# Optimization experiments

Hardware: AMD Instinct MI355X
Metric: run time of the kernel (lower is better)

## Reference

```python
import jax, jax.numpy as jnp
import numpy as np

B, S, D, H, NI, NB = 512, 200, 256, 4, 100000, 2
DH = D // H
NEG = float(-(2**32) + 1)
SCALE = float(1.0 / np.sqrt(DH))


def ln(x, g, b, eps=1e-3):
    # keras LayerNormalization (default epsilon=1e-3)
    m = jnp.mean(x, axis=-1, keepdims=True)
    v = jnp.var(x, axis=-1, keepdims=True)
    return (x - m) * jax.lax.rsqrt(v + eps) * g + b


def setup_inputs() -> dict:
    key = jax.random.key(0)
    ks = jax.random.split(key, 10)
    s = 0.02
    return {
        "input_ids": jax.random.randint(ks[0], (B, S), 0, NI + 1, dtype=jnp.int32),
        "item_emb": jax.random.normal(ks[1], (NI + 1, D), jnp.float32) * s,
        "pos_emb": jax.random.normal(ks[2], (S, D), jnp.float32) * s,
        "ln1_g": jnp.ones((NB, D), jnp.float32),
        "ln1_b": jnp.zeros((NB, D), jnp.float32),
        "wq": jax.random.normal(ks[3], (NB, D, D), jnp.float32) * s,
        "bq": jnp.zeros((NB, D), jnp.float32),
        "wk": jax.random.normal(ks[4], (NB, D, D), jnp.float32) * s,
        "bk": jnp.zeros((NB, D), jnp.float32),
        "wv": jax.random.normal(ks[5], (NB, D, D), jnp.float32) * s,
        "bv": jnp.zeros((NB, D), jnp.float32),
        "ln2_g": jnp.ones((NB, D), jnp.float32),
        "ln2_b": jnp.zeros((NB, D), jnp.float32),
        "wd": jax.random.normal(ks[6], (NB, D, D), jnp.float32) * s,
        "bd": jnp.zeros((NB, D), jnp.float32),
        "seq_g": jnp.ones((D,), jnp.float32),
        "seq_b": jnp.zeros((D,), jnp.float32),
        "out_item_emb": jax.random.normal(ks[7], (NI, D), jnp.float32) * s,
    }


def reference(input_ids, item_emb, pos_emb, ln1_g, ln1_b, wq, bq, wk, bk, wv, bv,
              ln2_g, ln2_b, wd, bd, seq_g, seq_b, out_item_emb):
    seq = item_emb[input_ids] + pos_emb[None]                      # [B,S,D]
    mask = (input_ids != NI).astype(seq.dtype)[:, :, None]        # pad id == num_items
    causal = jnp.tril(jnp.ones((S, S), bool))
    for i in range(NB):
        x = ln(seq, ln1_g[i], ln1_b[i])                            # queries (pre-norm)
        q = (x @ wq[i] + bq[i]).reshape(B, S, H, DH).transpose(0, 2, 1, 3)
        k = (seq @ wk[i] + bk[i]).reshape(B, S, H, DH).transpose(0, 2, 1, 3)
        v = (seq @ wv[i] + bv[i]).reshape(B, S, H, DH).transpose(0, 2, 1, 3)
        scores = jnp.einsum('bhqd,bhkd->bhqk', q, k) * SCALE       # [B,H,S,S]
        scores = jnp.where(causal, scores, NEG)
        attn = jax.nn.softmax(scores, axis=-1)
        o = jnp.einsum('bhqk,bhkd->bhqd', attn, v)
        o = o.transpose(0, 2, 1, 3).reshape(B, S, D)
        x2 = o + x                                                 # residual to normed queries
        y = jax.nn.relu(ln(x2, ln2_g[i], ln2_b[i]) @ wd[i] + bd[i])
        seq = (y + x2) * mask
    seq_emb = ln(seq[:, -1, :], seq_g, seq_b)                      # [B,D]
    return seq_emb @ out_item_emb.T                                # [B,num_items], linear act
```

## Files before the change

kernel.cpp:

```cpp
#include <hip/hip_runtime.h>
#include <hip/hip_bf16.h>
#include <cstdint>
#include <cstddef>

namespace {
constexpr int B = 512, S = 200, D = 256, H = 4, DH = 64, NI = 100000;
constexpr float EPS = 1e-3f;
constexpr float SCALE = 0.125f;
}

typedef __attribute__((ext_vector_type(8))) short bf16x8;
typedef __attribute__((ext_vector_type(4))) float f32x4;

__device__ inline unsigned short f2b(float f) {
  union { float f; unsigned int u; } v; v.f = f;
  unsigned int r = v.u + 0x7FFFu + ((v.u >> 16) & 1u);
  return (unsigned short)(r >> 16);
}

__device__ inline float b2f(unsigned short u) {
  union { unsigned int i; float f; } x; x.i = (unsigned int)u << 16; return x.f;
}

__device__ inline bf16x8 pack8(float4 a, float4 b) {
  bf16x8 r;
  r[0] = (short)f2b(a.x); r[1] = (short)f2b(a.y); r[2] = (short)f2b(a.z); r[3] = (short)f2b(a.w);
  r[4] = (short)f2b(b.x); r[5] = (short)f2b(b.y); r[6] = (short)f2b(b.z); r[7] = (short)f2b(b.w);
  return r;
}

__device__ inline ushort4 pack4(float4 a) {
  ushort4 r;
  r.x = f2b(a.x); r.y = f2b(a.y); r.z = f2b(a.z); r.w = f2b(a.w);
  return r;
}

__device__ inline float4 unpack4(ushort4 u) {
  float4 r; r.x = b2f(u.x); r.y = b2f(u.y); r.z = b2f(u.z); r.w = b2f(u.w); return r;
}

__device__ inline void gload_lds16(const unsigned short* g, unsigned short* l) {
  __builtin_amdgcn_global_load_lds((const __attribute__((address_space(1))) void*)g,
                                   (__attribute__((address_space(3))) void*)l, 16, 0, 0);
}

__global__ void cvt_wt_k(const float* __restrict__ wq, const float* __restrict__ wk,
                         const float* __restrict__ wv, const float* __restrict__ wd,
                         unsigned short* __restrict__ dst) {
  const int t = blockIdx.x * 256 + threadIdx.x;
  const int w = t >> 14, rem = t & 16383;
  const int k = rem >> 6, n4 = (rem & 63) * 4;
  const int blk = w >> 2, which = w & 3;
  const float* src = (which == 0 ? wq : which == 1 ? wk : which == 2 ? wv : wd) + blk * 65536;
  const float4 v = *(const float4*)(src + k * 256 + n4);
  unsigned short* d = dst + w * 65536;
  d[(n4 + 0) * 256 + k] = f2b(v.x);
  d[(n4 + 1) * 256 + k] = f2b(v.y);
  d[(n4 + 2) * 256 + k] = f2b(v.z);
  d[(n4 + 3) * 256 + k] = f2b(v.w);
}

__global__ __launch_bounds__(256) void embed_ln_k(const int* __restrict__ ids,
                                                  const float* __restrict__ ie,
                                                  const float* __restrict__ pe,
                                                  const float* __restrict__ g1,
                                                  const float* __restrict__ b1,
                                                  unsigned short* __restrict__ seq_bf,
                                                  unsigned short* __restrict__ x_bf) {
  const int row = blockIdx.x * 4 + (threadIdx.x >> 6);
  const int lane = threadIdx.x & 63;
  const int id = ids[row];
  const int s = row % S;
  float4 v = *(const float4*)(ie + (size_t)id * D + (lane << 2));
  const float4 p = *(const float4*)(pe + (size_t)s * D + (lane << 2));
  v.x += p.x; v.y += p.y; v.z += p.z; v.w += p.w;
  *(ushort4*)(seq_bf + (size_t)row * D + (lane << 2)) = pack4(v);
  const float4 vb = unpack4(pack4(v));
  float su = vb.x + vb.y + vb.z + vb.w;
  float ss = vb.x * vb.x + vb.y * vb.y + vb.z * vb.z + vb.w * vb.w;
#pragma unroll
  for (int off = 32; off; off >>= 1) {
    su += __shfl_xor(su, off);
    ss += __shfl_xor(ss, off);
  }
  const float mean = su * (1.f / D);
  const float rs = rsqrtf(ss * (1.f / D) - mean * mean + EPS);
  const float4 gv = *(const float4*)(g1 + (lane << 2));
  const float4 bv = *(const float4*)(b1 + (lane << 2));
  float4 o;
  o.x = (vb.x - mean) * rs * gv.x + bv.x;
  o.y = (vb.y - mean) * rs * gv.y + bv.y;
  o.z = (vb.z - mean) * rs * gv.z + bv.z;
  o.w = (vb.w - mean) * rs * gv.w + bv.w;
  *(ushort4*)(x_bf + (size_t)row * D + (lane << 2)) = pack4(o);
}

__global__ __launch_bounds__(256) void ln_bf_k(const unsigned short* __restrict__ in,
                                               size_t in_stride,
                                               const float* __restrict__ g, const float* __restrict__ b,
                                               unsigned short* __restrict__ outp, int nrows) {
  const int row = blockIdx.x * 4 + (threadIdx.x >> 6);
  if (row >= nrows) return;
  const int lane = threadIdx.x & 63;
  const float4 v = unpack4(*(const ushort4*)(in + (size_t)row * in_stride + (lane << 2)));
  float s = v.x + v.y + v.z + v.w;
  float ss = v.x * v.x + v.y * v.y + v.z * v.z + v.w * v.w;
#pragma unroll
  for (int off = 32; off; off >>= 1) {
    s += __shfl_xor(s, off);
    ss += __shfl_xor(ss, off);
  }
  const float mean = s * (1.f / D);
  const float rs = rsqrtf(ss * (1.f / D) - mean * mean + EPS);
  const float4 gv = *(const float4*)(g + (lane << 2));
  const float4 bv = *(const float4*)(b + (lane << 2));
  float4 o;
  o.x = (v.x - mean) * rs * gv.x + bv.x;
  o.y = (v.y - mean) * rs * gv.y + bv.y;
  o.z = (v.z - mean) * rs * gv.z + bv.z;
  o.w = (v.w - mean) * rs * gv.w + bv.w;
  *(ushort4*)(outp + (size_t)row * D + (lane << 2)) = pack4(o);
}

__global__ __launch_bounds__(256) void ln2x2_k(const unsigned short* __restrict__ x_bf,
                                               const unsigned short* __restrict__ o_bf,
                                               const float* __restrict__ g2, const float* __restrict__ b2,
                                               unsigned short* __restrict__ x2b,
                                               unsigned short* __restrict__ t_bf, int nrows) {
  const int row = blockIdx.x * 4 + (threadIdx.x >> 6);
  if (row >= nrows) return;
  const int lane = threadIdx.x & 63;
  const float4 xv = unpack4(*(const ushort4*)(x_bf + (size_t)row * D + (lane << 2)));
  const float4 ov = unpack4(*(const ushort4*)(o_bf + (size_t)row * D + (lane << 2)));
  float4 x2;
  x2.x = xv.x + ov.x; x2.y = xv.y + ov.y; x2.z = xv.z + ov.z; x2.w = xv.w + ov.w;
  *(ushort4*)(x2b + (size_t)row * D + (lane << 2)) = pack4(x2);
  float s2 = x2.x + x2.y + x2.z + x2.w;
  float ss2 = x2.x * x2.x + x2.y * x2.y + x2.z * x2.z + x2.w * x2.w;
#pragma unroll
  for (int off = 32; off; off >>= 1) {
    s2 += __shfl_xor(s2, off);
    ss2 += __shfl_xor(ss2, off);
  }
  const float mean2 = s2 * (1.f / D);
  const float rs2 = rsqrtf(ss2 * (1.f / D) - mean2 * mean2 + EPS);
  const float4 g2v = *(const float4*)(g2 + (lane << 2));
  const float4 b2v = *(const float4*)(b2 + (lane << 2));
  float4 t;
  t.x = (x2.x - mean2) * rs2 * g2v.x + b2v.x;
  t.y = (x2.y - mean2) * rs2 * g2v.y + b2v.y;
  t.z = (x2.z - mean2) * rs2 * g2v.z + b2v.z;
  t.w = (x2.w - mean2) * rs2 * g2v.w + b2v.w;
  *(ushort4*)(t_bf + (size_t)row * D + (lane << 2)) = pack4(t);
}

template <int RELU, int UPD, int LN1>
__global__ __launch_bounds__(512) void bgemm2_k(const unsigned short* __restrict__ A,
                                                const unsigned short* __restrict__ Wt,
                                                const float* __restrict__ bias,
                                                unsigned short* __restrict__ Cbf,
                                                const unsigned short* __restrict__ x2b,
                                                const int* __restrict__ ids, float osc,
                                                const float* __restrict__ g1,
                                                const float* __restrict__ b1,
                                                unsigned short* __restrict__ x1) {
  __shared__ unsigned short As[128 * 64];
  __shared__ unsigned short Bs[256 * 64];
  const int tid = threadIdx.x, w = tid >> 6, lane = tid & 63;
  const int kb = lane >> 4, ln = lane & 15;
  const int m0 = blockIdx.x * 128;
  const int wm = w & 1, wn = w >> 1;

  f32x4 acc[4][4];
#pragma unroll
  for (int i = 0; i < 4; ++i)
#pragma unroll
    for (int j = 0; j < 4; ++j) acc[i][j] = (f32x4){0.f, 0.f, 0.f, 0.f};

  for (int ks = 0; ks < 4; ++ks) {
    const int ko = ks * 64;
#pragma unroll
    for (int r = 0; r < 2; ++r) {
      const int g = (w * 2 + r) * 64 + lane;
      const int row = g >> 3, gc = g & 7;
      gload_lds16(A + (size_t)(m0 + row) * 256 + ko + ((gc ^ (row & 7)) << 3),
                  As + (size_t)(w * 2 + r) * 512);
    }
#pragma unroll
    for (int r = 0; r < 4; ++r) {
      const int g = (w * 4 + r) * 64 + lane;
      const int row = g >> 3, gc = g & 7;
      gload_lds16(Wt + (size_t)row * 256 + ko + ((gc ^ (row & 7)) << 3),
                  Bs + (size_t)(w * 4 + r) * 512);
    }
    __syncthreads();
#pragma unroll
    for (int h = 0; h < 2; ++h) {
      bf16x8 af[4], bfr[4];
#pragma unroll
      for (int i = 0; i < 4; ++i) {
        const int ar = wm * 64 + i * 16 + ln;
        af[i] = *(const bf16x8*)(As + ar * 64 + (((h * 64 + kb * 16) ^ ((ar & 7) << 4)) >> 1));
        const int br = wn * 64 + i * 16 + ln;
        bfr[i] = *(const bf16x8*)(Bs + br * 64 + (((h * 64 + kb * 16) ^ ((br & 7) << 4)) >> 1));
      }
#pragma unroll
      for (int i = 0; i < 4; ++i)
#pragma unroll
        for (int j = 0; j < 4; ++j)
          acc[i][j] = __builtin_amdgcn_mfma_f32_16x16x32_bf16(af[i], bfr[j], acc[i][j], 0, 0, 0);
    }
    __syncthreads();
  }

  const int crow0 = m0 + wm * 64 + kb * 4;
  const int ccol0 = wn * 64 + ln;
  float mk[4][4];
  if (UPD) {
#pragma unroll
    for (int i = 0; i < 4; ++i)
#pragma unroll
      for (int r = 0; r < 4; ++r) mk[i][r] = (ids[crow0 + i * 16 + r] != NI) ? 1.f : 0.f;
  }
#pragma unroll
  for (int j = 0; j < 4; ++j) {
    const int col = ccol0 + j * 16;
    const float bj = bias[col];
#pragma unroll
    for (int i = 0; i < 4; ++i) {
#pragma unroll
      for (int r = 0; r < 4; ++r) {
        const int row = crow0 + i * 16 + r;
        float v = (acc[i][j][r] + bj) * osc;
        if (RELU) v = fmaxf(v, 0.f);
        if (UPD) v = (v + b2f(x2b[(size_t)row * 256 + col])) * mk[i][r];
        const unsigned short vb = f2b(v);
        Cbf[(size_t)row * 256 + col] = vb;
        if (LN1) acc[i][j][r] = b2f(vb);
      }
    }
  }

  if (LN1) {
    float s_[4][4], ss_[4][4];
#pragma unroll
    for (int i = 0; i < 4; ++i)
#pragma unroll
      for (int r = 0; r < 4; ++r) {
        float s = 0.f, ss = 0.f;
#pragma unroll
        for (int j = 0; j < 4; ++j) { const float v = acc[i][j][r]; s += v; ss += v * v; }
#pragma unroll
        for (int off = 1; off < 16; off <<= 1) {
          s += __shfl_xor(s, off);
          ss += __shfl_xor(ss, off);
        }
        s_[i][r] = s; ss_[i][r] = ss;
      }
    float* red = (float*)As;
    if (ln == 0) {
#pragma unroll
      for (int i = 0; i < 4; ++i)
#pragma unroll
        for (int r = 0; r < 4; ++r) {
          const int rl = wm * 64 + kb * 4 + i * 16 + r;
          red[rl * 8 + wn * 2 + 0] = s_[i][r];
          red[rl * 8 + wn * 2 + 1] = ss_[i][r];
        }
    }
    __syncthreads();
#pragma unroll
    for (int i = 0; i < 4; ++i)
#pragma unroll
      for (int r = 0; r < 4; ++r) {
        const int rl = wm * 64 + kb * 4 + i * 16 + r;
        float S = 0.f, SS = 0.f;
#pragma unroll
        for (int q = 0; q < 4; ++q) { S += red[rl * 8 + q * 2]; SS += red[rl * 8 + q * 2 + 1]; }
        const float mean = S * (1.f / D);
        s_[i][r] = mean;
        ss_[i][r] = rsqrtf(SS * (1.f / D) - mean * mean + EPS);
      }
#pragma unroll
    for (int j = 0; j < 4; ++j) {
      const int col = ccol0 + j * 16;
      const float gc = g1[col], bc = b1[col];
#pragma unroll
      for (int i = 0; i < 4; ++i) {
#pragma unroll
        for (int r = 0; r < 4; ++r) {
          const int row = crow0 + i * 16 + r;
          const float xv = (acc[i][j][r] - s_[i][r]) * ss_[i][r] * gc + bc;
          x1[(size_t)row * 256 + col] = f2b(xv);
        }
      }
    }
  }
}

__global__ __launch_bounds__(256) void bgemm3_k(const unsigned short* __restrict__ A,
                                                const float* __restrict__ Wf,
                                                float* __restrict__ C, int M, int N) {
  __shared__ unsigned short As[128 * 64];
  __shared__ unsigned short Bs[128 * 64];
  const int tid = threadIdx.x, w = tid >> 6, lane = tid & 63;
  const int kb = lane >> 4, ln = lane & 15;
  const int m0 = blockIdx.x * 128;
  const int n0 = blockIdx.y * 128;
  const int wm = w & 1, wn = w >> 1;
  const int rl = lane >> 3;
  const int cb = (lane & 7) << 4;

  f32x4 acc[4][4];
#pragma unroll
  for (int i = 0; i < 4; ++i)
#pragma unroll
    for (int j = 0; j < 4; ++j) acc[i][j] = (f32x4){0.f, 0.f, 0.f, 0.f};

  for (int ks = 0; ks < 4; ++ks) {
    const int ko = ks * 64;
#pragma unroll
    for (int c = 0; c < 4; ++c) {
      const int arow = w * 32 + c * 8 + rl;
      const int sw = (arow & 7) << 4;
      const int cu = (cb ^ sw) >> 1;
      gload_lds16(A + (size_t)(m0 + arow) * 256 + ko + cu, As + (w * 32 + c * 8) * 64);
    }
#pragma unroll
    for (int c = 0; c < 4; ++c) {
      const int g = c * 256 + tid;
      const int row = g >> 3, gcs = g & 7;
      int br = n0 + row; if (br > N - 1) br = N - 1;
      const float* src = Wf + (size_t)br * 256 + ko + gcs * 8;
      const float4 f0 = *(const float4*)src;
      const float4 f1 = *(const float4*)(src + 4);
      *(bf16x8*)(Bs + row * 64 + ((gcs ^ (row & 7)) << 3)) = pack8(f0, f1);
    }
    __syncthreads();
#pragma unroll
    for (int h = 0; h < 2; ++h) {
      bf16x8 af[4], bfr[4];
#pragma unroll
      for (int i = 0; i < 4; ++i) {
        const int ar = wm * 64 + i * 16 + ln;
        af[i] = *(const bf16x8*)(As + ar * 64 + (((h * 64 + kb * 16) ^ ((ar & 7) << 4)) >> 1));
        const int br = wn * 64 + i * 16 + ln;
        bfr[i] = *(const bf16x8*)(Bs + br * 64 + (((h * 64 + kb * 16) ^ ((br & 7) << 4)) >> 1));
      }
#pragma unroll
      for (int i = 0; i < 4; ++i)
#pragma unroll
        for (int j = 0; j < 4; ++j)
          acc[i][j] = __builtin_amdgcn_mfma_f32_16x16x32_bf16(af[i], bfr[j], acc[i][j], 0, 0, 0);
    }
    __syncthreads();
  }

  const int crow0 = m0 + wm * 64 + kb * 4;
  const int ccol0 = n0 + wn * 64 + ln;
#pragma unroll
  for (int j = 0; j < 4; ++j) {
    const int col = ccol0 + j * 16;
    if (col >= N) continue;
#pragma unroll
    for (int i = 0; i < 4; ++i) {
#pragma unroll
      for (int r = 0; r < 4; ++r) {
        const int row = crow0 + i * 16 + r;
        C[(size_t)row * N + col] = acc[i][j][r];
      }
    }
  }
}

__global__ __launch_bounds__(256) void attn_k(const unsigned short* __restrict__ Q,
                                              const unsigned short* __restrict__ Kg,
                                              const unsigned short* __restrict__ Vg,
                                              unsigned short* __restrict__ O) {
  __shared__ unsigned short Ks[13312];
  __shared__ unsigned short Vt[13312];
  __shared__ unsigned short Ps[4 * 3328];
  const int b = blockIdx.x >> 2;
  const int h = blockIdx.x & 3;
  const int tid = threadIdx.x, w = tid >> 6, lane = tid & 63;
  const int kb = lane >> 4, ln = lane & 15;
  const size_t base = (size_t)b * S * D + h * DH;

  for (int s = w; s < 26; s += 4) {
    const int t = s >> 1, h2 = s & 1;
    int krow = t * 16 + ln; if (krow > S - 1) krow = S - 1;
    gload_lds16(Kg + base + (size_t)krow * D + h2 * 32 + kb * 8, Ks + s * 512);
  }
  for (int g = tid; g < 200 * 8; g += 256) {
    const int key = g >> 3, d0 = (g & 7) * 8;
    const bf16x8 v = *(const bf16x8*)(Vg + base + (size_t)key * D + d0);
#pragma unroll
    for (int i = 0; i < 8; ++i) {
      const int d = d0 + i, ct = d >> 4, cl = d & 15;
      int addr;
      if (key < 192) addr = (((ct * 6 + (key >> 5)) * 4 + ((key >> 3) & 3)) * 16 + cl) * 8 + (key & 7);
      else           addr = 12288 + ((ct * 2 + ((key >> 3) & 1)) * 16 + cl) * 8 + (key & 7);
      Vt[addr] = (unsigned short)v[i];
    }
  }
  if (tid < 64) {
    const int ct = tid >> 4, cl = tid & 15;
    *(bf16x8*)(Vt + 12288 + ((ct * 2 + 1) * 16 + cl) * 8) = (bf16x8)0;
  }
  __syncthreads();
  unsigned short* Pw = Ps + w * 3328;

#pragma unroll
  for (int it = 0; it < 4; ++it) {
    const int c = (it == 0) ? (12 - w) : (it == 1) ? (5 + w) : (it == 2) ? (4 - w)
                                                                         : (w == 3 ? 0 : -1);
    if (c < 0) continue;
    const int q0 = c << 4;
    const int tmax = (c | 1) > 12 ? 12 : (c | 1);
    const int ktm = c >> 1;

    int qr = q0 + ln; if (qr > S - 1) qr = S - 1;
    const unsigned short* qp = Q + base + (size_t)qr * D + kb * 8;
    const bf16x8 aq0 = *(const bf16x8*)(qp);
    const bf16x8 aq1 = *(const bf16x8*)(qp + 32);
    f32x4 sc[13];
#pragma unroll
    for (int t = 0; t < 13; ++t) {
      if (t <= tmax) {
        f32x4 a = {0.f, 0.f, 0.f, 0.f};
        a = __builtin_amdgcn_mfma_f32_16x16x32_bf16(aq0, *(const bf16x8*)(Ks + (t * 2 + 0) * 512 + lane * 8), a, 0, 0, 0);
        a = __builtin_amdgcn_mfma_f32_16x16x32_bf16(aq1, *(const bf16x8*)(Ks + (t * 2 + 1) * 512 + lane * 8), a, 0, 0, 0);
        sc[t] = a;
      }
    }
    float inv[4];
#pragma unroll
    for (int r = 0; r < 4; ++r) {
      const int q = q0 + kb * 4 + r;
      const int qrow = kb * 4 + r;
      float m = -1e30f;
#pragma unroll
      for (int t = 0; t < 13; ++t) {
        if (t <= tmax) {
          const int j = t * 16 + ln;
          float s = sc[t][r];
          s = (j <= q) ? s : -1e30f;
          sc[t][r] = s;
          m = fmaxf(m, s);
        }
      }
      m = fmaxf(m, __shfl_xor(m, 1));
      m = fmaxf(m, __shfl_xor(m, 2));
      m = fmaxf(m, __shfl_xor(m, 4));
      m = fmaxf(m, __shfl_xor(m, 8));
      float sm = 0.f;
#pragma unroll
      for (int t = 0; t < 13; ++t) {
        if (t <= tmax) {
          const float e = __expf(sc[t][r] - m);
          sm += e;
          int addr;
          if (t < 12) addr = (((t >> 1) * 4 + ((2 * t + (ln >> 3)) & 3)) * 16 + qrow) * 8 + (ln & 7);
          else        addr = 3072 + ((ln >> 3) * 16 + qrow) * 8 + (ln & 7);
          Pw[addr] = f2b(e);
        }
      }
      sm += __shfl_xor(sm, 1);
      sm += __shfl_xor(sm, 2);
      sm += __shfl_xor(sm, 4);
      sm += __shfl_xor(sm, 8);
      inv[r] = 1.f / sm;
    }
#pragma unroll
    for (int ct = 0; ct < 4; ++ct) {
      f32x4 a = {0.f, 0.f, 0.f, 0.f};
#pragma unroll
      for (int kt = 0; kt < 6; ++kt) {
        if (kt <= ktm) {
          const bf16x8 pa = *(const bf16x8*)(Pw + ((kt * 4 + kb) * 16 + ln) * 8);
          const bf16x8 vb = *(const bf16x8*)(Vt + (((ct * 6 + kt) * 4 + kb) * 16 + ln) * 8);
          a = __builtin_amdgcn_mfma_f32_16x16x32_bf16(pa, vb, a, 0, 0, 0);
        }
      }
      if (c == 12) {
        bf16x8 pa = (bf16x8)0, vb = (bf16x8)0;
        if (kb < 2) {
          pa = *(const bf16x8*)(Pw + 3072 + (kb * 16 + ln) * 8);
          vb = *(const bf16x8*)(Vt + 12288 + ((ct * 2 + kb) * 16 + ln) * 8);
        }
        a = __builtin_amdgcn_mfma_f32_16x16x32_bf16(pa, vb, a, 0, 0, 0);
      }
#pragma unroll
      for (int r = 0; r < 4; ++r) {
        const int q = q0 + kb * 4 + r;
        if (q < S) O[base + (size_t)q * D + ct * 16 + ln] = f2b(a[r] * inv[r]);
      }
    }
  }
}

extern "C" void kernel_launch(void* const* d_in, const int* in_sizes, int n_in,
                              void* d_out, int out_size, void* d_ws, size_t ws_size,
                              hipStream_t stream) {
  const int* ids        = (const int*)d_in[0];
  const float* item_emb = (const float*)d_in[1];
  const float* pos_emb  = (const float*)d_in[2];
  const float* ln1_g    = (const float*)d_in[3];
  const float* ln1_b    = (const float*)d_in[4];
  const float* wq       = (const float*)d_in[5];
  const float* bq       = (const float*)d_in[6];
  const float* wk       = (const float*)d_in[7];
  const float* bk       = (const float*)d_in[8];
  const float* wv       = (const float*)d_in[9];
  const float* bv       = (const float*)d_in[10];
  const float* ln2_g    = (const float*)d_in[11];
  const float* ln2_b    = (const float*)d_in[12];
  const float* wd       = (const float*)d_in[13];
  const float* bd       = (const float*)d_in[14];
  const float* seq_g    = (const float*)d_in[15];
  const float* seq_b    = (const float*)d_in[16];
  const float* w_out    = (const float*)d_in[17];
  float* out = (float*)d_out;

  char* wsb = (char*)d_ws;
  unsigned short* seq_bf = (unsigned short*)(wsb + 0);
  unsigned short* x_bf   = (unsigned short*)(wsb + 52428800);
  unsigned short* q_bf   = (unsigned short*)(wsb + 104857600);
  unsigned short* k_bf   = (unsigned short*)(wsb + 157286400);
  unsigned short* v_bf   = (unsigned short*)(wsb + 209715200);
  unsigned short* o_bf   = (unsigned short*)(wsb + 262144000);
  unsigned short* x2b    = (unsigned short*)(wsb + 314572800);
  unsigned short* wtb    = (unsigned short*)(wsb + 367001600);
  unsigned short* semb   = (unsigned short*)(wsb + 368050176);

  const int M = B * S;
  const int ln_grid = (M + 3) / 4;

  cvt_wt_k<<<512, 256, 0, stream>>>(wq, wk, wv, wd, wtb);
  embed_ln_k<<<ln_grid, 256, 0, stream>>>(ids, item_emb, pos_emb, ln1_g, ln1_b, seq_bf, x_bf);

  for (int blk = 0; blk < 2; ++blk) {
    const float* l2g = ln2_g + blk * D;
    const float* l2b = ln2_b + blk * D;
    const unsigned short* WT = wtb + (size_t)blk * 4 * 65536;

    bgemm2_k<0, 0, 0><<<800, 512, 0, stream>>>(seq_bf, WT + 1 * 65536, bk + blk * D, k_bf,
                                               nullptr, nullptr, 1.f, nullptr, nullptr, nullptr);
    bgemm2_k<0, 0, 0><<<800, 512, 0, stream>>>(seq_bf, WT + 2 * 65536, bv + blk * D, v_bf,
                                               nullptr, nullptr, 1.f, nullptr, nullptr, nullptr);
    bgemm2_k<0, 0, 0><<<800, 512, 0, stream>>>(x_bf, WT + 0 * 65536, bq + blk * D, q_bf,
                                               nullptr, nullptr, SCALE, nullptr, nullptr, nullptr);
    attn_k<<<B * H, 256, 0, stream>>>(q_bf, k_bf, v_bf, o_bf);
    ln2x2_k<<<ln_grid, 256, 0, stream>>>(x_bf, o_bf, l2g, l2b, x2b, q_bf, M);
    if (blk == 0) {
      bgemm2_k<1, 1, 1><<<800, 512, 0, stream>>>(q_bf, WT + 3 * 65536, bd + blk * D, seq_bf,
                                                 x2b, ids, 1.f, ln1_g + D, ln1_b + D, x_bf);
    } else {
      bgemm2_k<1, 1, 0><<<800, 512, 0, stream>>>(q_bf, WT + 3 * 65536, bd + blk * D, seq_bf,
                                                 x2b, ids, 1.f, nullptr, nullptr, nullptr);
    }
  }

  ln_bf_k<<<(B + 3) / 4, 256, 0, stream>>>(seq_bf + (size_t)(S - 1) * D, (size_t)S * D,
                                           seq_g, seq_b, semb, B);
  bgemm3_k<<<dim3(4, 782), 256, 0, stream>>>(semb, w_out, out, B, NI);
}
```

Baseline: 780.7 us.

## Fuse residual and LN2 into FFN GEMM; restructure logits GEMM to load weights once

The separate residual-add and LayerNorm-2 kernel is folded into a new FFN kernel. That kernel builds x2 = x + o for a 64-row tile in shared memory, normalizes it in place, and then runs the dense GEMM with the ReLU, residual, mask and optional next LN1 epilogue. This removes the x2 and t intermediates from global memory and one launch per block. The output-projection GEMM is also restructured so that each block converts a 128-row slice of the fp32 item embedding to bf16 once and loops over all 512 batch rows. Previously each weight tile was re-read and re-converted for each of four M tiles. The new kernels use much larger shared memory, 128 KB for the logits kernel, which lowers occupancy.

```diff
diff --git a/kernel.cpp b/kernel.cpp
--- a/kernel.cpp
+++ b/kernel.cpp
@@ -122,48 +122,10 @@
   *(ushort4*)(outp + (size_t)row * D + (lane << 2)) = pack4(o);
 }
 
-__global__ __launch_bounds__(256) void ln2x2_k(const unsigned short* __restrict__ x_bf,
-                                               const unsigned short* __restrict__ o_bf,
-                                               const float* __restrict__ g2, const float* __restrict__ b2,
-                                               unsigned short* __restrict__ x2b,
-                                               unsigned short* __restrict__ t_bf, int nrows) {
-  const int row = blockIdx.x * 4 + (threadIdx.x >> 6);
-  if (row >= nrows) return;
-  const int lane = threadIdx.x & 63;
-  const float4 xv = unpack4(*(const ushort4*)(x_bf + (size_t)row * D + (lane << 2)));
-  const float4 ov = unpack4(*(const ushort4*)(o_bf + (size_t)row * D + (lane << 2)));
-  float4 x2;
-  x2.x = xv.x + ov.x; x2.y = xv.y + ov.y; x2.z = xv.z + ov.z; x2.w = xv.w + ov.w;
-  *(ushort4*)(x2b + (size_t)row * D + (lane << 2)) = pack4(x2);
-  float s2 = x2.x + x2.y + x2.z + x2.w;
-  float ss2 = x2.x * x2.x + x2.y * x2.y + x2.z * x2.z + x2.w * x2.w;
-#pragma unroll
-  for (int off = 32; off; off >>= 1) {
-    s2 += __shfl_xor(s2, off);
-    ss2 += __shfl_xor(ss2, off);
-  }
-  const float mean2 = s2 * (1.f / D);
-  const float rs2 = rsqrtf(ss2 * (1.f / D) - mean2 * mean2 + EPS);
-  const float4 g2v = *(const float4*)(g2 + (lane << 2));
-  const float4 b2v = *(const float4*)(b2 + (lane << 2));
-  float4 t;
-  t.x = (x2.x - mean2) * rs2 * g2v.x + b2v.x;
-  t.y = (x2.y - mean2) * rs2 * g2v.y + b2v.y;
-  t.z = (x2.z - mean2) * rs2 * g2v.z + b2v.z;
-  t.w = (x2.w - mean2) * rs2 * g2v.w + b2v.w;
-  *(ushort4*)(t_bf + (size_t)row * D + (lane << 2)) = pack4(t);
-}
-
-template <int RELU, int UPD, int LN1>
 __global__ __launch_bounds__(512) void bgemm2_k(const unsigned short* __restrict__ A,
                                                 const unsigned short* __restrict__ Wt,
                                                 const float* __restrict__ bias,
-                                                unsigned short* __restrict__ Cbf,
-                                                const unsigned short* __restrict__ x2b,
-                                                const int* __restrict__ ids, float osc,
-                                                const float* __restrict__ g1,
-                                                const float* __restrict__ b1,
-                                                unsigned short* __restrict__ x1) {
+                                                unsigned short* __restrict__ Cbf, float osc) {
   __shared__ unsigned short As[128 * 64];
   __shared__ unsigned short Bs[256 * 64];
   const int tid = threadIdx.x, w = tid >> 6, lane = tid & 63;
@@ -215,13 +177,6 @@
 
   const int crow0 = m0 + wm * 64 + kb * 4;
   const int ccol0 = wn * 64 + ln;
-  float mk[4][4];
-  if (UPD) {
-#pragma unroll
-    for (int i = 0; i < 4; ++i)
-#pragma unroll
-      for (int r = 0; r < 4; ++r) mk[i][r] = (ids[crow0 + i * 16 + r] != NI) ? 1.f : 0.f;
-  }
 #pragma unroll
   for (int j = 0; j < 4; ++j) {
     const int col = ccol0 + j * 16;
@@ -231,16 +186,156 @@
 #pragma unroll
       for (int r = 0; r < 4; ++r) {
         const int row = crow0 + i * 16 + r;
-        float v = (acc[i][j][r] + bj) * osc;
-        if (RELU) v = fmaxf(v, 0.f);
-        if (UPD) v = (v + b2f(x2b[(size_t)row * 256 + col])) * mk[i][r];
+        Cbf[(size_t)row * 256 + col] = f2b((acc[i][j][r] + bj) * osc);
+      }
+    }
+  }
+}
+
+template <int LN1>
+__global__ __launch_bounds__(256) void ffn_k(const unsigned short* __restrict__ x_bf,
+                                             const unsigned short* __restrict__ o_bf,
+                                             const unsigned short* __restrict__ Wt,
+                                             const float* __restrict__ bias,
+                                             const float* __restrict__ g2,
+                                             const float* __restrict__ b2,
+                                             const int* __restrict__ ids,
+                                             unsigned short* __restrict__ seq_out,
+                                             const float* __restrict__ g1,
+                                             const float* __restrict__ b1,
+                                             unsigned short* __restrict__ x1) {
+  __shared__ unsigned short Xt[64 * 256];
+  __shared__ unsigned short Bs[256 * 64];
+  __shared__ float stats[64][2];
+  __shared__ float params[512];
+  const int tid = threadIdx.x, w = tid >> 6, lane = tid & 63;
+  const int kb = lane >> 4, ln = lane & 15;
+  const int m0 = blockIdx.x * 64;
+  const int wn = w;
+
+  params[tid] = g2[tid & 255];
+  params[256 + (tid & 255)] = b2[tid & 255];
+#pragma unroll
+  for (int it = 0; it < 8; ++it) {
+    const int g = it * 256 + tid;
+    const int row = g >> 5, gc = g & 31;
+    const bf16x8 xv = *(const bf16x8*)(x_bf + (size_t)(m0 + row) * 256 + gc * 8);
+    const bf16x8 ov = *(const bf16x8*)(o_bf + (size_t)(m0 + row) * 256 + gc * 8);
+    bf16x8 sv;
+#pragma unroll
+    for (int e = 0; e < 8; ++e)
+      sv[e] = (short)f2b(b2f((unsigned short)xv[e]) + b2f((unsigned short)ov[e]));
+    *(bf16x8*)(Xt + row * 256 + (((gc * 16) ^ ((row & 7) << 4)) >> 1)) = sv;
+  }
+  __syncthreads();
+  {
+    const int srow = tid >> 2, sq = tid & 3;
+    float su = 0.f, ssq = 0.f;
+#pragma unroll
+    for (int gg = 0; gg < 8; ++gg) {
+      const int gc = sq * 8 + gg;
+      const bf16x8 v = *(const bf16x8*)(Xt + srow * 256 + (((gc * 16) ^ ((srow & 7) << 4)) >> 1));
+#pragma unroll
+      for (int e = 0; e < 8; ++e) {
+        const float f = b2f((unsigned short)v[e]);
+        su += f; ssq += f * f;
+      }
+    }
+    su += __shfl_xor(su, 1); ssq += __shfl_xor(ssq, 1);
+    su += __shfl_xor(su, 2); ssq += __shfl_xor(ssq, 2);
+    if (sq == 0) {
+      const float mean = su * (1.f / D);
+      stats[srow][0] = mean;
+      stats[srow][1] = rsqrtf(ssq * (1.f / D) - mean * mean + EPS);
+    }
+  }
+  __syncthreads();
+  float ep[4][4][4];
+  const int ccl = wn * 64 + ln;
+#pragma unroll
+  for (int i = 0; i < 4; ++i)
+#pragma unroll
+    for (int j = 0; j < 4; ++j)
+#pragma unroll
+      for (int r = 0; r < 4; ++r) {
+        const int rr = i * 16 + kb * 4 + r;
+        const int col = ccl + j * 16;
+        ep[i][j][r] = b2f(Xt[rr * 256 + (((col * 2) ^ ((rr & 7) << 4)) >> 1)]);
+      }
+  __syncthreads();
+#pragma unroll
+  for (int it = 0; it < 8; ++it) {
+    const int g = it * 256 + tid;
+    const int row = g >> 5, gc = g & 31;
+    const int idx = row * 256 + (((gc * 16) ^ ((row & 7) << 4)) >> 1);
+    const bf16x8 v = *(const bf16x8*)(Xt + idx);
+    const float mu = stats[row][0], rs = stats[row][1];
+    bf16x8 t;
+#pragma unroll
+    for (int e = 0; e < 8; ++e) {
+      const int k = gc * 8 + e;
+      t[e] = (short)f2b((b2f((unsigned short)v[e]) - mu) * rs * params[k] + params[256 + k]);
+    }
+    *(bf16x8*)(Xt + idx) = t;
+  }
+  __syncthreads();
+  f32x4 acc[4][4];
+#pragma unroll
+  for (int i = 0; i < 4; ++i)
+#pragma unroll
+    for (int j = 0; j < 4; ++j) acc[i][j] = (f32x4){0.f, 0.f, 0.f, 0.f};
+
+  for (int ks = 0; ks < 4; ++ks) {
+#pragma unroll
+    for (int r = 0; r < 8; ++r) {
+      const int g = (w * 8 + r) * 64 + lane;
+      const int row = g >> 3, gc = g & 7;
+      gload_lds16(Wt + (size_t)row * 256 + ks * 64 + ((gc ^ (row & 7)) << 3),
+                  Bs + (size_t)(w * 8 + r) * 512);
+    }
+    __syncthreads();
+#pragma unroll
+    for (int h = 0; h < 2; ++h) {
+      bf16x8 af[4], bfr[4];
+#pragma unroll
+      for (int i = 0; i < 4; ++i) {
+        const int ar = i * 16 + ln;
+        af[i] = *(const bf16x8*)(Xt + ar * 256 +
+                                 ((ks * 128 + ((h * 64 + kb * 16) ^ ((ar & 7) << 4))) >> 1));
+        const int br = wn * 64 + i * 16 + ln;
+        bfr[i] = *(const bf16x8*)(Bs + br * 64 + (((h * 64 + kb * 16) ^ ((br & 7) << 4)) >> 1));
+      }
+#pragma unroll
+      for (int i = 0; i < 4; ++i)
+#pragma unroll
+        for (int j = 0; j < 4; ++j)
+          acc[i][j] = __builtin_amdgcn_mfma_f32_16x16x32_bf16(af[i], bfr[j], acc[i][j], 0, 0, 0);
+    }
+    __syncthreads();
+  }
+  float mk[4][4];
+#pragma unroll
+  for (int i = 0; i < 4; ++i)
+#pragma unroll
+    for (int r = 0; r < 4; ++r)
+      mk[i][r] = (ids[m0 + i * 16 + kb * 4 + r] != NI) ? 1.f : 0.f;
+#pragma unroll
+  for (int j = 0; j < 4; ++j) {
+    const int col = ccl + j * 16;
+    const float bj = bias[col];
+#pragma unroll
+    for (int i = 0; i < 4; ++i) {
+#pragma unroll
+      for (int r = 0; r < 4; ++r) {
+        const int grow = m0 + i * 16 + kb * 4 + r;
+        float v = fmaxf(acc[i][j][r] + bj, 0.f);
+        v = (v + ep[i][j][r]) * mk[i][r];
         const unsigned short vb = f2b(v);
-        Cbf[(size_t)row * 256 + col] = vb;
+        seq_out[(size_t)grow * 256 + col] = vb;
         if (LN1) acc[i][j][r] = b2f(vb);
       }
     }
   }
-
   if (LN1) {
     float s_[4][4], ss_[4][4];
 #pragma unroll
@@ -257,15 +352,16 @@
         }
         s_[i][r] = s; ss_[i][r] = ss;
       }
-    float* red = (float*)As;
+    float* red = params;
+    __syncthreads();
     if (ln == 0) {
 #pragma unroll
       for (int i = 0; i < 4; ++i)
 #pragma unroll
         for (int r = 0; r < 4; ++r) {
-          const int rl = wm * 64 + kb * 4 + i * 16 + r;
-          red[rl * 8 + wn * 2 + 0] = s_[i][r];
-          red[rl * 8 + wn * 2 + 1] = ss_[i][r];
+          const int rt = i * 16 + kb * 4 + r;
+          red[rt * 8 + wn * 2 + 0] = s_[i][r];
+          red[rt * 8 + wn * 2 + 1] = ss_[i][r];
         }
     }
     __syncthreads();
@@ -273,103 +369,102 @@
     for (int i = 0; i < 4; ++i)
 #pragma unroll
       for (int r = 0; r < 4; ++r) {
-        const int rl = wm * 64 + kb * 4 + i * 16 + r;
-        float S = 0.f, SS = 0.f;
-#pragma unroll
-        for (int q = 0; q < 4; ++q) { S += red[rl * 8 + q * 2]; SS += red[rl * 8 + q * 2 + 1]; }
-        const float mean = S * (1.f / D);
+        const int rt = i * 16 + kb * 4 + r;
+        float Sv = 0.f, SS = 0.f;
+#pragma unroll
+        for (int q = 0; q < 4; ++q) { Sv += red[rt * 8 + q * 2]; SS += red[rt * 8 + q * 2 + 1]; }
+        const float mean = Sv * (1.f / D);
         s_[i][r] = mean;
         ss_[i][r] = rsqrtf(SS * (1.f / D) - mean * mean + EPS);
       }
 #pragma unroll
     for (int j = 0; j < 4; ++j) {
+      const int col = ccl + j * 16;
+      const float gc = g1[col], bc = b1[col];
+#pragma unroll
+      for (int i = 0; i < 4; ++i) {
+#pragma unroll
+        for (int r = 0; r < 4; ++r) {
+          const int grow = m0 + i * 16 + kb * 4 + r;
+          const float xv = (acc[i][j][r] - s_[i][r]) * ss_[i][r] * gc + bc;
+          x1[(size_t)grow * 256 + col] = f2b(xv);
+        }
+      }
+    }
+  }
+}
+
+__global__ __launch_bounds__(256) void logits_k(const unsigned short* __restrict__ A,
+                                                const float* __restrict__ Wf,
+                                                float* __restrict__ C) {
+  __shared__ unsigned short Bs[128 * 256];
+  __shared__ unsigned short As[128 * 256];
+  const int tid = threadIdx.x, w = tid >> 6, lane = tid & 63;
+  const int kb = lane >> 4, ln = lane & 15;
+  const int wm = w & 1, wn = w >> 1;
+  const int n0 = blockIdx.x * 128;
+#pragma unroll
+  for (int it = 0; it < 16; ++it) {
+    const int g = it * 256 + tid;
+    const int row = g >> 5, gc = g & 31;
+    int br = n0 + row; if (br > NI - 1) br = NI - 1;
+    const float* src = Wf + (size_t)br * 256 + gc * 8;
+    const float4 f0 = *(const float4*)src;
+    const float4 f1 = *(const float4*)(src + 4);
+    *(bf16x8*)(Bs + row * 256 + (((gc * 16) ^ ((row & 7) << 4)) >> 1)) = pack8(f0, f1);
+  }
+  for (int m = 0; m < 4; ++m) {
+    const int m0 = m * 128;
+#pragma unroll
+    for (int it = 0; it < 16; ++it) {
+      const int g = it * 256 + w * 64 + lane;
+      const int row = g >> 5, gc = g & 31;
+      gload_lds16(A + (size_t)(m0 + row) * 256 + (((gc * 16) ^ ((row & 7) << 4)) >> 1),
+                  As + (size_t)(it * 256 + w * 64) * 8);
+    }
+    __syncthreads();
+    f32x4 acc[4][4];
+#pragma unroll
+    for (int i = 0; i < 4; ++i)
+#pragma unroll
+      for (int j = 0; j < 4; ++j) acc[i][j] = (f32x4){0.f, 0.f, 0.f, 0.f};
+#pragma unroll
+    for (int ks = 0; ks < 4; ++ks) {
+#pragma unroll
+      for (int h = 0; h < 2; ++h) {
+        bf16x8 af[4], bfr[4];
+#pragma unroll
+        for (int i = 0; i < 4; ++i) {
+          const int ar = wm * 64 + i * 16 + ln;
+          af[i] = *(const bf16x8*)(As + ar * 256 +
+                                   ((ks * 128 + ((h * 64 + kb * 16) ^ ((ar & 7) << 4))) >> 1));
+          const int br = wn * 64 + i * 16 + ln;
+          bfr[i] = *(const bf16x8*)(Bs + br * 256 +
+                                    ((ks * 128 + ((h * 64 + kb * 16) ^ ((br & 7) << 4))) >> 1));
+        }
+#pragma unroll
+        for (int i = 0; i < 4; ++i)
+#pragma unroll
+          for (int j = 0; j < 4; ++j)
+            acc[i][j] = __builtin_amdgcn_mfma_f32_16x16x32_bf16(af[i], bfr[j], acc[i][j], 0, 0, 0);
+      }
+    }
+    const int crow0 = m0 + wm * 64 + kb * 4;
+    const int ccol0 = n0 + wn * 64 + ln;
+#pragma unroll
+    for (int j = 0; j < 4; ++j) {
       const int col = ccol0 + j * 16;
-      const float gc = g1[col], bc = b1[col];
+      if (col >= NI) continue;
 #pragma unroll
       for (int i = 0; i < 4; ++i) {
 #pragma unroll
         for (int r = 0; r < 4; ++r) {
           const int row = crow0 + i * 16 + r;
-          const float xv = (acc[i][j][r] - s_[i][r]) * ss_[i][r] * gc + bc;
-          x1[(size_t)row * 256 + col] = f2b(xv);
-        }
-      }
-    }
-  }
-}
-
-__global__ __launch_bounds__(256) void bgemm3_k(const unsigned short* __restrict__ A,
-                                                const float* __restrict__ Wf,
-                                                float* __restrict__ C, int M, int N) {
-  __shared__ unsigned short As[128 * 64];
-  __shared__ unsigned short Bs[128 * 64];
-  const int tid = threadIdx.x, w = tid >> 6, lane = tid & 63;
-  const int kb = lane >> 4, ln = lane & 15;
-  const int m0 = blockIdx.x * 128;
-  const int n0 = blockIdx.y * 128;
-  const int wm = w & 1, wn = w >> 1;
-  const int rl = lane >> 3;
-  const int cb = (lane & 7) << 4;
-
-  f32x4 acc[4][4];
-#pragma unroll
-  for (int i = 0; i < 4; ++i)
-#pragma unroll
-    for (int j = 0; j < 4; ++j) acc[i][j] = (f32x4){0.f, 0.f, 0.f, 0.f};
-
-  for (int ks = 0; ks < 4; ++ks) {
-    const int ko = ks * 64;
-#pragma unroll
-    for (int c = 0; c < 4; ++c) {
-      const int arow = w * 32 + c * 8 + rl;
-      const int sw = (arow & 7) << 4;
-      const int cu = (cb ^ sw) >> 1;
-      gload_lds16(A + (size_t)(m0 + arow) * 256 + ko + cu, As + (w * 32 + c * 8) * 64);
-    }
-#pragma unroll
-    for (int c = 0; c < 4; ++c) {
-      const int g = c * 256 + tid;
-      const int row = g >> 3, gcs = g & 7;
-      int br = n0 + row; if (br > N - 1) br = N - 1;
-      const float* src = Wf + (size_t)br * 256 + ko + gcs * 8;
-      const float4 f0 = *(const float4*)src;
-      const float4 f1 = *(const float4*)(src + 4);
-      *(bf16x8*)(Bs + row * 64 + ((gcs ^ (row & 7)) << 3)) = pack8(f0, f1);
-    }
-    __syncthreads();
-#pragma unroll
-    for (int h = 0; h < 2; ++h) {
-      bf16x8 af[4], bfr[4];
-#pragma unroll
-      for (int i = 0; i < 4; ++i) {
-        const int ar = wm * 64 + i * 16 + ln;
-        af[i] = *(const bf16x8*)(As + ar * 64 + (((h * 64 + kb * 16) ^ ((ar & 7) << 4)) >> 1));
-        const int br = wn * 64 + i * 16 + ln;
-        bfr[i] = *(const bf16x8*)(Bs + br * 64 + (((h * 64 + kb * 16) ^ ((br & 7) << 4)) >> 1));
-      }
-#pragma unroll
-      for (int i = 0; i < 4; ++i)
-#pragma unroll
-        for (int j = 0; j < 4; ++j)
-          acc[i][j] = __builtin_amdgcn_mfma_f32_16x16x32_bf16(af[i], bfr[j], acc[i][j], 0, 0, 0);
-    }
-    __syncthreads();
-  }
-
-  const int crow0 = m0 + wm * 64 + kb * 4;
-  const int ccol0 = n0 + wn * 64 + ln;
-#pragma unroll
-  for (int j = 0; j < 4; ++j) {
-    const int col = ccol0 + j * 16;
-    if (col >= N) continue;
-#pragma unroll
-    for (int i = 0; i < 4; ++i) {
-#pragma unroll
-      for (int r = 0; r < 4; ++r) {
-        const int row = crow0 + i * 16 + r;
-        C[(size_t)row * N + col] = acc[i][j][r];
-      }
-    }
+          C[(size_t)row * NI + col] = acc[i][j][r];
+        }
+      }
+    }
+    __syncthreads();
   }
 }
 
@@ -529,9 +624,8 @@
   unsigned short* k_bf   = (unsigned short*)(wsb + 157286400);
   unsigned short* v_bf   = (unsigned short*)(wsb + 209715200);
   unsigned short* o_bf   = (unsigned short*)(wsb + 262144000);
-  unsigned short* x2b    = (unsigned short*)(wsb + 314572800);
-  unsigned short* wtb    = (unsigned short*)(wsb + 367001600);
-  unsigned short* semb   = (unsigned short*)(wsb + 368050176);
+  unsigned short* wtb    = (unsigned short*)(wsb + 314572800);
+  unsigned short* semb   = (unsigned short*)(wsb + 315621376);
 
   const int M = B * S;
   const int ln_grid = (M + 3) / 4;
@@ -540,28 +634,24 @@
   embed_ln_k<<<ln_grid, 256, 0, stream>>>(ids, item_emb, pos_emb, ln1_g, ln1_b, seq_bf, x_bf);
 
   for (int blk = 0; blk < 2; ++blk) {
-    const float* l2g = ln2_g + blk * D;
-    const float* l2b = ln2_b + blk * D;
     const unsigned short* WT = wtb + (size_t)blk * 4 * 65536;
 
-    bgemm2_k<0, 0, 0><<<800, 512, 0, stream>>>(seq_bf, WT + 1 * 65536, bk + blk * D, k_bf,
-                                               nullptr, nullptr, 1.f, nullptr, nullptr, nullptr);
-    bgemm2_k<0, 0, 0><<<800, 512, 0, stream>>>(seq_bf, WT + 2 * 65536, bv + blk * D, v_bf,
-                                               nullptr, nullptr, 1.f, nullptr, nullptr, nullptr);
-    bgemm2_k<0, 0, 0><<<800, 512, 0, stream>>>(x_bf, WT + 0 * 65536, bq + blk * D, q_bf,
-                                               nullptr, nullptr, SCALE, nullptr, nullptr, nullptr);
+    bgemm2_k<<<800, 512, 0, stream>>>(seq_bf, WT + 1 * 65536, bk + blk * D, k_bf, 1.f);
+    bgemm2_k<<<800, 512, 0, stream>>>(seq_bf, WT + 2 * 65536, bv + blk * D, v_bf, 1.f);
+    bgemm2_k<<<800, 512, 0, stream>>>(x_bf, WT + 0 * 65536, bq + blk * D, q_bf, SCALE);
     attn_k<<<B * H, 256, 0, stream>>>(q_bf, k_bf, v_bf, o_bf);
-    ln2x2_k<<<ln_grid, 256, 0, stream>>>(x_bf, o_bf, l2g, l2b, x2b, q_bf, M);
     if (blk == 0) {
-      bgemm2_k<1, 1, 1><<<800, 512, 0, stream>>>(q_bf, WT + 3 * 65536, bd + blk * D, seq_bf,
-                                                 x2b, ids, 1.f, ln1_g + D, ln1_b + D, x_bf);
+      ffn_k<1><<<1600, 256, 0, stream>>>(x_bf, o_bf, WT + 3 * 65536, bd + blk * D,
+                                         ln2_g + blk * D, ln2_b + blk * D, ids, seq_bf,
+                                         ln1_g + D, ln1_b + D, x_bf);
     } else {
-      bgemm2_k<1, 1, 0><<<800, 512, 0, stream>>>(q_bf, WT + 3 * 65536, bd + blk * D, seq_bf,
-                                                 x2b, ids, 1.f, nullptr, nullptr, nullptr);
+      ffn_k<0><<<1600, 256, 0, stream>>>(x_bf, o_bf, WT + 3 * 65536, bd + blk * D,
+                                         ln2_g + blk * D, ln2_b + blk * D, ids, seq_bf,
+                                         nullptr, nullptr, nullptr);
     }
   }
 
   ln_bf_k<<<(B + 3) / 4, 256, 0, stream>>>(seq_bf + (size_t)(S - 1) * D, (size_t)S * D,
                                            seq_g, seq_b, semb, B);
-  bgemm3_k<<<dim3(4, 782), 256, 0, stream>>>(semb, w_out, out, B, NI);
-}
+  logits_k<<<782, 256, 0, stream>>>(semb, w_out, out);
+}
```

Result: faster. 737.5 us (median of 2 runs) (-5.5%).
